# Kernel tuning notes

Hardware: AMD Instinct MI355X
Metric: run time of the kernel (lower is better)

The kernel has to match this reference:

```python
import jax, jax.numpy as jnp
import numpy as np

B, S, E, H = 8, 1024, 1024, 16
D = E // H  # head_dim = 64


def setup_inputs() -> dict:
    rng = jax.random.key(0)
    ks = jax.random.split(rng, 12)
    sc = 1.0 / np.sqrt(E).astype(np.float32)
    rows = jnp.broadcast_to(jnp.arange(S)[:, None], (S, S)).astype(jnp.int32)
    cols = jnp.broadcast_to(jnp.arange(S)[None, :], (S, S)).astype(jnp.int32)
    return {
        "query": jax.random.normal(ks[0], (B, S, E), jnp.float32),
        "key": jax.random.normal(ks[1], (B, S, E), jnp.float32),
        "value": jax.random.normal(ks[2], (B, S, E), jnp.float32),
        # per-head q/k/v projections stacked on a leading head axis [H, E, D]
        "Wq": jax.random.normal(ks[3], (H, E, D), jnp.float32) * sc,
        "bq": jnp.zeros((H, D), jnp.float32),
        "Wk": jax.random.normal(ks[4], (H, E, D), jnp.float32) * sc,
        "bk": jnp.zeros((H, D), jnp.float32),
        "Wv": jax.random.normal(ks[5], (H, E, D), jnp.float32) * sc,
        "bv": jnp.zeros((H, D), jnp.float32),
        "Wo": jax.random.normal(ks[6], (E, E), jnp.float32) * sc,
        "bo": jnp.zeros((E,), jnp.float32),
        # learned 2D position-bias table, gathered via index pair -> [S, S]
        "position_bias": jax.random.normal(ks[7], (S, S), jnp.float32) * 0.02,
        "pb_idx0": rows,
        "pb_idx1": cols,
        # causal mask: True entries are masked (filled with -inf)
        "mask": jnp.triu(jnp.ones((S, S), jnp.bool_), k=1),
    }


def reference(query, key, value, Wq, bq, Wk, bk, Wv, bv, Wo, bo,
              position_bias, pb_idx0, pb_idx1, mask):
    # batched per-head projections (equivalent to the per-head Linear loop)
    q = jnp.einsum("bse,hed->bhsd", query, Wq) + bq[None, :, None, :]
    k = jnp.einsum("bse,hed->bhsd", key, Wk) + bk[None, :, None, :]
    v = jnp.einsum("bse,hed->bhsd", value, Wv) + bv[None, :, None, :]
    # scaled dot-product logits [B, H, S, S]
    logits = jnp.einsum("bhqd,bhkd->bhqk", q, k) / jnp.sqrt(jnp.float32(D))
    logits = logits + position_bias[pb_idx0, pb_idx1]  # additive bias, shared across heads
    logits = jnp.where(mask, -jnp.inf, logits)  # masked_fill
    attn = jax.nn.softmax(logits, axis=-1)
    out = jnp.einsum("bhqk,bhkd->bhqd", attn, v)
    out = out.transpose(0, 2, 1, 3).reshape(out.shape[0], out.shape[2], H * D)  # join heads
    return out @ Wo + bo  # output_embedding
```

## Files before the change

kernel.cpp:

```cpp
#include <hip/hip_runtime.h>

typedef unsigned short u16;
typedef unsigned int u32;
typedef short s16x8 __attribute__((ext_vector_type(8)));
typedef float f32x4 __attribute__((ext_vector_type(4)));

#define BB 8
#define SS 1024
#define EE 1024
#define HH 16
#define DD 64

__device__ inline u16 f2bf(float f) {
  union { float f; unsigned u; } x; x.f = f;
  unsigned r = x.u + 0x7fffu + ((x.u >> 16) & 1u);
  return (u16)(r >> 16);
}
__device__ inline float bf2f(u16 u) {
  union { unsigned u; float f; } x; x.u = ((unsigned)u) << 16; return x.f;
}
__device__ inline u32 cvtpk(float lo, float hi) {
  u32 r;
  asm("v_cvt_pk_bf16_f32 %0, %1, %2" : "=v"(r) : "v"(lo), "v"(hi));
  return r;
}

__global__ __launch_bounds__(256) void transpose_w(
    const float* __restrict__ Wq, const float* __restrict__ Wk,
    const float* __restrict__ Wv, const float* __restrict__ Wo,
    u16* __restrict__ Wt3, u16* __restrict__ Wot)
{
  __shared__ float tile[64][65];
  int z = blockIdx.z;
  const float* src; u16* dst; int r0, c0, ldS, ldD;
  if (z < 3) {
    const float* W = (z == 0) ? Wq : (z == 1) ? Wk : Wv;
    int h = blockIdx.y;
    src = W + h * (EE * DD); r0 = blockIdx.x * 64; c0 = 0; ldS = DD;
    dst = Wt3 + z * (EE * EE) + h * 64 * EE; ldD = EE;
  } else {
    src = Wo; r0 = blockIdx.x * 64; c0 = blockIdx.y * 64; ldS = EE;
    dst = Wot; ldD = EE;
  }
  int t = threadIdx.x;
  int lr = t >> 2, lc = (t & 3) * 16;
#pragma unroll
  for (int i = 0; i < 16; i += 4) {
    float4 f = *(const float4*)(src + (size_t)(r0 + lr) * ldS + c0 + lc + i);
    tile[lr][lc + i] = f.x; tile[lr][lc + i + 1] = f.y;
    tile[lr][lc + i + 2] = f.z; tile[lr][lc + i + 3] = f.w;
  }
  __syncthreads();
#pragma unroll
  for (int i = 0; i < 16; i++)
    dst[(size_t)(c0 + lr) * ldD + r0 + lc + i] = f2bf(tile[lc + i][lr]);
}

__global__ __launch_bounds__(256) void pb2h(const float* __restrict__ pb,
                                            u16* __restrict__ pbh)
{
  int t = blockIdx.x * 256 + threadIdx.x;
  pbh[t] = f2bf(pb[t]);
}

__global__ __launch_bounds__(256) void f2h(const float* __restrict__ in,
                                           u16* __restrict__ out)
{
  int i = (blockIdx.x * 256 + threadIdx.x) * 8;
  float4 a = *(const float4*)(in + i);
  float4 b = *(const float4*)(in + i + 4);
  uint4 r;
  r.x = cvtpk(a.x, a.y); r.y = cvtpk(a.z, a.w);
  r.z = cvtpk(b.x, b.y); r.w = cvtpk(b.z, b.w);
  *(uint4*)(out + i) = r;
}

#define BK 64
__global__ __launch_bounds__(256, 2) void gemm128(
    const u16* __restrict__ At, const u16* __restrict__ Bt,
    const float* __restrict__ bias, void* __restrict__ out,
    int M, int N, int K, int mode)
{
  __shared__ __attribute__((aligned(16))) u16 As[128 * BK];
  __shared__ __attribute__((aligned(16))) u16 Bs[128 * BK];
  int t = threadIdx.x;
  int lane = t & 63, wid = t >> 6;
  int row0 = blockIdx.y * 128, col0 = blockIdx.x * 128;
  int wr = (wid >> 1) * 64, wc = (wid & 1) * 64;
  int lr = lane & 15, lg = lane >> 4;
  f32x4 acc[4][4];
#pragma unroll
  for (int m = 0; m < 4; m++)
#pragma unroll
    for (int n = 0; n < 4; n++)
      acc[m][n] = (f32x4){0.f, 0.f, 0.f, 0.f};

  int grow[4], gls[4];
#pragma unroll
  for (int j = 0; j < 4; j++) {
    int c = wid * 256 + j * 64 + lane;
    grow[j] = c >> 3;
    gls[j] = (c & 7) ^ (grow[j] & 7);
  }

  for (int k0 = 0; k0 < K; k0 += BK) {
    __syncthreads();
#pragma unroll
    for (int j = 0; j < 4; j++) {
      __builtin_amdgcn_global_load_lds(
          (const u32*)(At + (size_t)(row0 + grow[j]) * K + k0 + gls[j] * 8),
          (u32*)((char*)As + (wid * 256 + j * 64) * 16), 16, 0, 0);
      __builtin_amdgcn_global_load_lds(
          (const u32*)(Bt + (size_t)(col0 + grow[j]) * K + k0 + gls[j] * 8),
          (u32*)((char*)Bs + (wid * 256 + j * 64) * 16), 16, 0, 0);
    }
    __syncthreads();
#pragma unroll
    for (int kf = 0; kf < 2; kf++) {
      s16x8 af[4], bf[4];
#pragma unroll
      for (int m = 0; m < 4; m++) {
        int r = wr + m * 16 + lr;
        af[m] = *(const s16x8*)((char*)As + r * 128 + (((kf * 4 + lg) ^ (r & 7)) * 16));
      }
#pragma unroll
      for (int n = 0; n < 4; n++) {
        int r = wc + n * 16 + lr;
        bf[n] = *(const s16x8*)((char*)Bs + r * 128 + (((kf * 4 + lg) ^ (r & 7)) * 16));
      }
#pragma unroll
      for (int m = 0; m < 4; m++)
#pragma unroll
        for (int n = 0; n < 4; n++)
          acc[m][n] = __builtin_amdgcn_mfma_f32_16x16x32_bf16(af[m], bf[n], acc[m][n], 0, 0, 0);
    }
  }

#pragma unroll
  for (int n = 0; n < 4; n++) {
    int colb = col0 + wc + n * 16 + lr;
    float bv = bias[colb];
#pragma unroll
    for (int m = 0; m < 4; m++) {
#pragma unroll
      for (int v = 0; v < 4; v++) {
        int rowb = row0 + wr + m * 16 + lg * 4 + v;
        float val = acc[m][n][v] + bv;
        if (mode == 3) {
          ((float*)out)[(size_t)rowb * N + colb] = val;
        } else {
          int bb = rowb >> 10, s = rowb & 1023, hh = colb >> 6, dd = colb & 63;
          u16 u = f2bf(val);
          if (mode == 2)
            ((u16*)out)[(size_t)((bb * HH + hh) * DD + dd) * SS + s] = u;
          else
            ((u16*)out)[(size_t)((bb * HH + hh) * SS + s) * DD + dd] = u;
        }
      }
    }
  }
}

#define KVB 64
#define KS_OFF 0
#define VS_OFF 8192
#define PW_OFF 16384

__global__ __launch_bounds__(256) void attn_k(
    const u16* __restrict__ qp, const u16* __restrict__ kp,
    const u16* __restrict__ vT, const u16* __restrict__ pbh,
    u16* __restrict__ attout)
{
  __shared__ __attribute__((aligned(16))) char lds[32768];
  int wgid = blockIdx.x;
  int bh = (wgid & 7) * 16 + ((wgid >> 3) & 15);
  int s8 = 7 - (wgid >> 7);
  int t = threadIdx.x;
  int lane = t & 63, wid = t >> 6;
  int lr = lane & 15, lg = lane >> 4;
  const char* Qb = (const char*)(qp + (size_t)bh * SS * DD);
  const char* Kb = (const char*)(kp + (size_t)bh * SS * DD);
  const char* Vb = (const char*)(vT + (size_t)bh * SS * DD);
  int b = bh >> 4, h = bh & 15;
  char* Pbase = lds + PW_OFF + wid * 4096;

  int q0b = s8 * 128;
  int q0 = q0b + wid * 32;
  int kv_end = q0 + 32;

  s16x8 qf[2][2];
#pragma unroll
  for (int m = 0; m < 2; m++)
#pragma unroll
    for (int kf = 0; kf < 2; kf++)
      qf[m][kf] = *(const s16x8*)(Qb + (size_t)(q0 + m * 16 + lr) * 128 + kf * 64 + lg * 16);

  f32x4 o[2][4];
  float mrun[2][4], lrun[2][4];
#pragma unroll
  for (int m = 0; m < 2; m++) {
#pragma unroll
    for (int n = 0; n < 4; n++) o[m][n] = (f32x4){0.f, 0.f, 0.f, 0.f};
#pragma unroll
    for (int v = 0; v < 4; v++) { mrun[m][v] = -1e30f; lrun[m][v] = 0.f; }
  }

  for (int kv0 = 0; kv0 < q0b + 128; kv0 += KVB) {
#pragma unroll
    for (int i = 0; i < 2; i++) {
      int c = i * 256 + t;
      int row = c >> 3, colb = (c & 7) << 4;
      int sw = (row & 7) << 4;
      uint4 kd = *(const uint4*)(Kb + (size_t)(kv0 + row) * 128 + colb);
      uint4 vd = *(const uint4*)(Vb + (size_t)row * 2048 + (size_t)kv0 * 2 + colb);
      *(uint4*)(lds + KS_OFF + row * 128 + (colb ^ sw)) = kd;
      *(uint4*)(lds + VS_OFF + row * 128 + (colb ^ sw)) = vd;
    }
    __syncthreads();

    if (kv0 < kv_end) {
      f32x4 s[2][4];
#pragma unroll
      for (int tt = 0; tt < 4; tt++) {
        int r = tt * 16 + lr;
        int sw = (r & 7) << 4;
        s16x8 k0 = *(const s16x8*)(lds + KS_OFF + (((r << 7) + lg * 16) ^ sw));
        s16x8 k1 = *(const s16x8*)(lds + KS_OFF + (((r << 7) + 64 + lg * 16) ^ sw));
#pragma unroll
        for (int m = 0; m < 2; m++) {
          f32x4 acc = (f32x4){0.f, 0.f, 0.f, 0.f};
          acc = __builtin_amdgcn_mfma_f32_16x16x32_bf16(qf[m][0], k0, acc, 0, 0, 0);
          acc = __builtin_amdgcn_mfma_f32_16x16x32_bf16(qf[m][1], k1, acc, 0, 0, 0);
          s[m][tt] = acc;
        }
      }
      bool full = (kv0 + KVB - 1 <= q0);
#pragma unroll
      for (int m = 0; m < 2; m++) {
#pragma unroll
        for (int v = 0; v < 4; v++) {
          int qq = q0 + m * 16 + lg * 4 + v;
          const u16* pbrow = pbh + (size_t)qq * SS + kv0 + lr;
          float sv[4];
#pragma unroll
          for (int tt = 0; tt < 4; tt++) {
            float bi = bf2f(pbrow[tt * 16]);
            float x = fmaf(s[m][tt][v], 0.125f, bi);
            if (!full && (kv0 + tt * 16 + lr > qq)) x = -1e30f;
            sv[tt] = x;
          }
          float mt = fmaxf(fmaxf(sv[0], sv[1]), fmaxf(sv[2], sv[3]));
          mt = fmaxf(mt, __shfl_xor(mt, 1));
          mt = fmaxf(mt, __shfl_xor(mt, 2));
          mt = fmaxf(mt, __shfl_xor(mt, 4));
          mt = fmaxf(mt, __shfl_xor(mt, 8));
          float mn = fmaxf(mrun[m][v], mt);
          float corr = __expf(mrun[m][v] - mn);
          float p0 = __expf(sv[0] - mn);
          float p1 = __expf(sv[1] - mn);
          float p2 = __expf(sv[2] - mn);
          float p3 = __expf(sv[3] - mn);
          float rs = (p0 + p1) + (p2 + p3);
          rs += __shfl_xor(rs, 1);
          rs += __shfl_xor(rs, 2);
          rs += __shfl_xor(rs, 4);
          rs += __shfl_xor(rs, 8);
          lrun[m][v] = lrun[m][v] * corr + rs;
          mrun[m][v] = mn;
#pragma unroll
          for (int n = 0; n < 4; n++) o[m][n][v] *= corr;
          int qrow = m * 16 + lg * 4 + v;
          int rb = qrow * 128;
          int sw = (qrow & 7) << 4;
          *(u16*)(Pbase + ((rb + (lr * 2)) ^ sw))       = f2bf(p0);
          *(u16*)(Pbase + ((rb + 32 + (lr * 2)) ^ sw))  = f2bf(p1);
          *(u16*)(Pbase + ((rb + 64 + (lr * 2)) ^ sw))  = f2bf(p2);
          *(u16*)(Pbase + ((rb + 96 + (lr * 2)) ^ sw))  = f2bf(p3);
        }
      }
#pragma unroll
      for (int kf = 0; kf < 2; kf++) {
        s16x8 pf[2], vf[4];
#pragma unroll
        for (int m = 0; m < 2; m++) {
          int r = m * 16 + lr;
          pf[m] = *(const s16x8*)(Pbase + ((r * 128 + kf * 64 + lg * 16) ^ ((r & 7) << 4)));
        }
#pragma unroll
        for (int n = 0; n < 4; n++) {
          int r = n * 16 + lr;
          vf[n] = *(const s16x8*)(lds + VS_OFF + (((r << 7) + kf * 64 + lg * 16) ^ ((r & 7) << 4)));
        }
#pragma unroll
        for (int m = 0; m < 2; m++)
#pragma unroll
          for (int n = 0; n < 4; n++)
            o[m][n] = __builtin_amdgcn_mfma_f32_16x16x32_bf16(pf[m], vf[n], o[m][n], 0, 0, 0);
      }
    }
    __syncthreads();
  }

#pragma unroll
  for (int m = 0; m < 2; m++)
#pragma unroll
    for (int v = 0; v < 4; v++) {
      int qq = q0 + m * 16 + lg * 4 + v;
      float inv = 1.0f / lrun[m][v];
#pragma unroll
      for (int n = 0; n < 4; n++)
        attout[(size_t)(b * SS + qq) * EE + h * DD + n * 16 + lr] = f2bf(o[m][n][v] * inv);
    }
}

extern "C" void kernel_launch(void* const* d_in, const int* in_sizes, int n_in,
                              void* d_out, int out_size, void* d_ws, size_t ws_size,
                              hipStream_t stream) {
  const float* query = (const float*)d_in[0];
  const float* key   = (const float*)d_in[1];
  const float* value = (const float*)d_in[2];
  const float* Wq = (const float*)d_in[3];
  const float* bq = (const float*)d_in[4];
  const float* Wk = (const float*)d_in[5];
  const float* bk = (const float*)d_in[6];
  const float* Wv = (const float*)d_in[7];
  const float* bv = (const float*)d_in[8];
  const float* Wo = (const float*)d_in[9];
  const float* bo = (const float*)d_in[10];
  const float* pb = (const float*)d_in[11];

  char* ws = (char*)d_ws;
  u16* att  = (u16*)(ws + 0);
  u16* Wt3  = (u16*)(ws + 16777216);
  u16* Wot  = (u16*)(ws + 23068672);
  u16* qp   = (u16*)(ws + 25165824);
  u16* kp   = (u16*)(ws + 41943040);
  u16* vT   = (u16*)(ws + 58720256);
  u16* pbh  = Wt3;

  transpose_w<<<dim3(16, 16, 4), 256, 0, stream>>>(Wq, Wk, Wv, Wo, Wt3, Wot);

  f2h<<<dim3(4096), 256, 0, stream>>>(key, att);
  gemm128<<<dim3(8, 64), 256, 0, stream>>>(att, Wt3 + EE * EE, bk, kp, BB * SS, EE, EE, 1);
  f2h<<<dim3(4096), 256, 0, stream>>>(query, att);
  gemm128<<<dim3(8, 64), 256, 0, stream>>>(att, Wt3, bq, qp, BB * SS, EE, EE, 0);
  f2h<<<dim3(4096), 256, 0, stream>>>(value, att);
  gemm128<<<dim3(8, 64), 256, 0, stream>>>(att, Wt3 + 2 * EE * EE, bv, vT, BB * SS, EE, EE, 2);

  pb2h<<<dim3(SS * SS / 256), 256, 0, stream>>>(pb, pbh);

  attn_k<<<dim3(1024), 256, 0, stream>>>(qp, kp, vT, pbh, att);

  gemm128<<<dim3(8, 64), 256, 0, stream>>>(att, Wot, bo, d_out, BB * SS, EE, EE, 3);
}
```

Before: 228.4 us.

## Fuse fp32-to-bf16 input conversion into projection GEMMs and skip redundant softmax rescales

The projection GEMM now reads fp32 activations directly, converts them to bf16 in registers and stores them into swizzled LDS. This removes three separate conversion kernels and their global round trip. The attention kernel also skips the running-max correction (exp and rescale of the accumulators) when no lane's max increased. The trade-off is that the A-tile fp32 loads are synchronous register loads instead of async global-to-LDS loads, which may reduce overlap inside the GEMM.

Measured after the change: 340.6 us. 1.49x slower.

```diff
diff --git a/kernel.cpp b/kernel.cpp
--- a/kernel.cpp
+++ b/kernel.cpp
@@ -63,23 +63,11 @@
   pbh[t] = f2bf(pb[t]);
 }
 
-__global__ __launch_bounds__(256) void f2h(const float* __restrict__ in,
-                                           u16* __restrict__ out)
-{
-  int i = (blockIdx.x * 256 + threadIdx.x) * 8;
-  float4 a = *(const float4*)(in + i);
-  float4 b = *(const float4*)(in + i + 4);
-  uint4 r;
-  r.x = cvtpk(a.x, a.y); r.y = cvtpk(a.z, a.w);
-  r.z = cvtpk(b.x, b.y); r.w = cvtpk(b.z, b.w);
-  *(uint4*)(out + i) = r;
-}
-
 #define BK 64
 __global__ __launch_bounds__(256, 2) void gemm128(
-    const u16* __restrict__ At, const u16* __restrict__ Bt,
+    const void* __restrict__ Ain, const u16* __restrict__ Bt,
     const float* __restrict__ bias, void* __restrict__ out,
-    int M, int N, int K, int mode)
+    int M, int N, int K, int mode, int a_f32)
 {
   __shared__ __attribute__((aligned(16))) u16 As[128 * BK];
   __shared__ __attribute__((aligned(16))) u16 Bs[128 * BK];
@@ -102,14 +90,35 @@
     grow[j] = c >> 3;
     gls[j] = (c & 7) ^ (grow[j] & 7);
   }
+  int sr = t >> 1, ss = (t & 1) * 4;
+  const float* Af = (const float*)Ain + (size_t)(row0 + sr) * K + ss * 8;
+  const u16* Ab16 = (const u16*)Ain;
 
   for (int k0 = 0; k0 < K; k0 += BK) {
+    uint4 aw[4];
+    if (a_f32) {
+#pragma unroll
+      for (int j = 0; j < 4; j++) {
+        float4 fa = *(const float4*)(Af + k0 + j * 8);
+        float4 fb = *(const float4*)(Af + k0 + j * 8 + 4);
+        aw[j].x = cvtpk(fa.x, fa.y); aw[j].y = cvtpk(fa.z, fa.w);
+        aw[j].z = cvtpk(fb.x, fb.y); aw[j].w = cvtpk(fb.z, fb.w);
+      }
+    }
     __syncthreads();
+    if (a_f32) {
+#pragma unroll
+      for (int j = 0; j < 4; j++)
+        *(uint4*)((char*)As + sr * 128 + (((ss + j) ^ (sr & 7)) * 16)) = aw[j];
+    } else {
+#pragma unroll
+      for (int j = 0; j < 4; j++)
+        __builtin_amdgcn_global_load_lds(
+            (const u32*)(Ab16 + (size_t)(row0 + grow[j]) * K + k0 + gls[j] * 8),
+            (u32*)((char*)As + (wid * 256 + j * 64) * 16), 16, 0, 0);
+    }
 #pragma unroll
     for (int j = 0; j < 4; j++) {
-      __builtin_amdgcn_global_load_lds(
-          (const u32*)(At + (size_t)(row0 + grow[j]) * K + k0 + gls[j] * 8),
-          (u32*)((char*)As + (wid * 256 + j * 64) * 16), 16, 0, 0);
       __builtin_amdgcn_global_load_lds(
           (const u32*)(Bt + (size_t)(col0 + grow[j]) * K + k0 + gls[j] * 8),
           (u32*)((char*)Bs + (wid * 256 + j * 64) * 16), 16, 0, 0);
@@ -255,7 +264,13 @@
           mt = fmaxf(mt, __shfl_xor(mt, 4));
           mt = fmaxf(mt, __shfl_xor(mt, 8));
           float mn = fmaxf(mrun[m][v], mt);
-          float corr = __expf(mrun[m][v] - mn);
+          if (__any(mt > mrun[m][v])) {
+            float corr = __expf(mrun[m][v] - mn);
+            lrun[m][v] *= corr;
+#pragma unroll
+            for (int n = 0; n < 4; n++) o[m][n][v] *= corr;
+          }
+          mrun[m][v] = mn;
           float p0 = __expf(sv[0] - mn);
           float p1 = __expf(sv[1] - mn);
           float p2 = __expf(sv[2] - mn);
@@ -265,10 +280,7 @@
           rs += __shfl_xor(rs, 2);
           rs += __shfl_xor(rs, 4);
           rs += __shfl_xor(rs, 8);
-          lrun[m][v] = lrun[m][v] * corr + rs;
-          mrun[m][v] = mn;
-#pragma unroll
-          for (int n = 0; n < 4; n++) o[m][n][v] *= corr;
+          lrun[m][v] += rs;
           int qrow = m * 16 + lg * 4 + v;
           int rb = qrow * 128;
           int sw = (qrow & 7) << 4;
@@ -340,16 +352,13 @@
 
   transpose_w<<<dim3(16, 16, 4), 256, 0, stream>>>(Wq, Wk, Wv, Wo, Wt3, Wot);
 
-  f2h<<<dim3(4096), 256, 0, stream>>>(key, att);
-  gemm128<<<dim3(8, 64), 256, 0, stream>>>(att, Wt3 + EE * EE, bk, kp, BB * SS, EE, EE, 1);
-  f2h<<<dim3(4096), 256, 0, stream>>>(query, att);
-  gemm128<<<dim3(8, 64), 256, 0, stream>>>(att, Wt3, bq, qp, BB * SS, EE, EE, 0);
-  f2h<<<dim3(4096), 256, 0, stream>>>(value, att);
-  gemm128<<<dim3(8, 64), 256, 0, stream>>>(att, Wt3 + 2 * EE * EE, bv, vT, BB * SS, EE, EE, 2);
+  gemm128<<<dim3(8, 64), 256, 0, stream>>>(query, Wt3,            bq, qp, BB * SS, EE, EE, 0, 1);
+  gemm128<<<dim3(8, 64), 256, 0, stream>>>(key,   Wt3 + EE * EE,  bk, kp, BB * SS, EE, EE, 1, 1);
+  gemm128<<<dim3(8, 64), 256, 0, stream>>>(value, Wt3 + 2 * EE * EE, bv, vT, BB * SS, EE, EE, 2, 1);
 
   pb2h<<<dim3(SS * SS / 256), 256, 0, stream>>>(pb, pbh);
 
   attn_k<<<dim3(1024), 256, 0, stream>>>(qp, kp, vT, pbh, att);
 
-  gemm128<<<dim3(8, 64), 256, 0, stream>>>(att, Wot, bo, d_out, BB * SS, EE, EE, 3);
-}
+  gemm128<<<dim3(8, 64), 256, 0, stream>>>(att, Wot, bo, d_out, BB * SS, EE, EE, 3, 0);
+}
```

## Double-buffer K/V tiles in LDS with register prefetch in attention kernel

Applied to the files above, without the earlier changes.

Converts the attention kernel's K/V staging into a two-buffer scheme. Global loads for the next KV tile go into registers before the current tile's QK/softmax/PV work and are written to the alternate LDS buffer afterwards, so one barrier per iteration is removed and load latency overlaps compute. LDS use grows from 32KB to 48KB and register pressure rises, which may reduce occupancy.

Result: slower. 250.9 us (+9.8%).

```diff
diff --git a/kernel.cpp b/kernel.cpp
--- a/kernel.cpp
+++ b/kernel.cpp
@@ -164,14 +164,15 @@
 #define KVB 64
 #define KS_OFF 0
 #define VS_OFF 8192
-#define PW_OFF 16384
+#define BUF_STRIDE 16384
+#define PW_OFF 32768
 
 __global__ __launch_bounds__(256) void attn_k(
     const u16* __restrict__ qp, const u16* __restrict__ kp,
     const u16* __restrict__ vT, const u16* __restrict__ pbh,
     u16* __restrict__ attout)
 {
-  __shared__ __attribute__((aligned(16))) char lds[32768];
+  __shared__ __attribute__((aligned(16))) char lds[49152];
   int wgid = blockIdx.x;
   int bh = (wgid & 7) * 16 + ((wgid >> 3) & 15);
   int s8 = 7 - (wgid >> 7);
@@ -188,6 +189,13 @@
   int q0 = q0b + wid * 32;
   int kv_end = q0 + 32;
 
+  int srow[2], scolb[2], ssw[2];
+#pragma unroll
+  for (int i = 0; i < 2; i++) {
+    int c = i * 256 + t;
+    srow[i] = c >> 3; scolb[i] = (c & 7) << 4; ssw[i] = (srow[i] & 7) << 4;
+  }
+
   s16x8 qf[2][2];
 #pragma unroll
   for (int m = 0; m < 2; m++)
@@ -205,18 +213,33 @@
     for (int v = 0; v < 4; v++) { mrun[m][v] = -1e30f; lrun[m][v] = 0.f; }
   }
 
-  for (int kv0 = 0; kv0 < q0b + 128; kv0 += KVB) {
-#pragma unroll
-    for (int i = 0; i < 2; i++) {
-      int c = i * 256 + t;
-      int row = c >> 3, colb = (c & 7) << 4;
-      int sw = (row & 7) << 4;
-      uint4 kd = *(const uint4*)(Kb + (size_t)(kv0 + row) * 128 + colb);
-      uint4 vd = *(const uint4*)(Vb + (size_t)row * 2048 + (size_t)kv0 * 2 + colb);
-      *(uint4*)(lds + KS_OFF + row * 128 + (colb ^ sw)) = kd;
-      *(uint4*)(lds + VS_OFF + row * 128 + (colb ^ sw)) = vd;
-    }
-    __syncthreads();
+  int ntiles = (q0b + 128) / KVB;
+
+#pragma unroll
+  for (int i = 0; i < 2; i++) {
+    uint4 kd = *(const uint4*)(Kb + (size_t)srow[i] * 128 + scolb[i]);
+    uint4 vd = *(const uint4*)(Vb + (size_t)srow[i] * 2048 + scolb[i]);
+    *(uint4*)(lds + KS_OFF + srow[i] * 128 + (scolb[i] ^ ssw[i])) = kd;
+    *(uint4*)(lds + VS_OFF + srow[i] * 128 + (scolb[i] ^ ssw[i])) = vd;
+  }
+  __syncthreads();
+
+  int cur = 0;
+  for (int ti = 0; ti < ntiles; ti++) {
+    int kv0 = ti * KVB;
+    bool pref = (ti + 1 < ntiles);
+    uint4 kd[2], vd[2];
+    if (pref) {
+      int kvn = kv0 + KVB;
+#pragma unroll
+      for (int i = 0; i < 2; i++) {
+        kd[i] = *(const uint4*)(Kb + (size_t)(kvn + srow[i]) * 128 + scolb[i]);
+        vd[i] = *(const uint4*)(Vb + (size_t)srow[i] * 2048 + (size_t)kvn * 2 + scolb[i]);
+      }
+    }
+
+    const char* Kcur = lds + cur * BUF_STRIDE + KS_OFF;
+    const char* Vcur = lds + cur * BUF_STRIDE + VS_OFF;
 
     if (kv0 < kv_end) {
       f32x4 s[2][4];
@@ -224,8 +247,8 @@
       for (int tt = 0; tt < 4; tt++) {
         int r = tt * 16 + lr;
         int sw = (r & 7) << 4;
-        s16x8 k0 = *(const s16x8*)(lds + KS_OFF + (((r << 7) + lg * 16) ^ sw));
-        s16x8 k1 = *(const s16x8*)(lds + KS_OFF + (((r << 7) + 64 + lg * 16) ^ sw));
+        s16x8 k0 = *(const s16x8*)(Kcur + (((r << 7) + lg * 16) ^ sw));
+        s16x8 k1 = *(const s16x8*)(Kcur + (((r << 7) + 64 + lg * 16) ^ sw));
 #pragma unroll
         for (int m = 0; m < 2; m++) {
           f32x4 acc = (f32x4){0.f, 0.f, 0.f, 0.f};
@@ -289,7 +312,7 @@
 #pragma unroll
         for (int n = 0; n < 4; n++) {
           int r = n * 16 + lr;
-          vf[n] = *(const s16x8*)(lds + VS_OFF + (((r << 7) + kf * 64 + lg * 16) ^ ((r & 7) << 4)));
+          vf[n] = *(const s16x8*)(Vcur + (((r << 7) + kf * 64 + lg * 16) ^ ((r & 7) << 4)));
         }
 #pragma unroll
         for (int m = 0; m < 2; m++)
@@ -298,7 +321,17 @@
             o[m][n] = __builtin_amdgcn_mfma_f32_16x16x32_bf16(pf[m], vf[n], o[m][n], 0, 0, 0);
       }
     }
+
+    if (pref) {
+      char* dst = lds + (cur ^ 1) * BUF_STRIDE;
+#pragma unroll
+      for (int i = 0; i < 2; i++) {
+        *(uint4*)(dst + KS_OFF + srow[i] * 128 + (scolb[i] ^ ssw[i])) = kd[i];
+        *(uint4*)(dst + VS_OFF + srow[i] * 128 + (scolb[i] ^ ssw[i])) = vd[i];
+      }
+    }
     __syncthreads();
+    cur ^= 1;
   }
 
 #pragma unroll
```
